# Performance work log

Measured on AMD Instinct MI355X. Metric: run time of the kernel, lower is better.

## Reference

```python
import jax, jax.numpy as jnp
import numpy as np
from jax import lax

IN_CH, OC, NUM_LAYER = 6, 16, 256
ENC_DIM = OC * 4  # 64
DECODE_LEN = 23
FLAT = 5184


def _conv3d(x, w, b):
    # x: (B,C,D,H,W), w: (O,I,3,3,3), padding 1, stride 1
    y = lax.conv_general_dilated(x, w, window_strides=(1, 1, 1),
                                 padding=((1, 1), (1, 1), (1, 1)),
                                 dimension_numbers=('NCDHW', 'OIDHW', 'NCDHW'))
    return y + b[None, :, None, None, None]


def _maxpool(x):
    # MaxPool3d kernel (2,2,1) stride (2,2,1) over (D,H,W)
    return lax.reduce_window(x, -jnp.inf, lax.max,
                             (1, 1, 2, 2, 1), (1, 1, 2, 2, 1), 'VALID')


def setup_inputs() -> dict:
    key = jax.random.key(0)
    ks = jax.random.split(key, 24)
    n = lambda k, s: jax.random.normal(k, s, dtype=jnp.float32) * 0.05
    z = lambda s: jnp.zeros(s, dtype=jnp.float32)
    return {
        'x': jax.random.normal(ks[0], (512, IN_CH, 24, 72, 3), dtype=jnp.float32),
        'w1': n(ks[1], (OC, IN_CH, 3, 3, 3)), 'b1': z((OC,)),
        'w2': n(ks[2], (OC * 2, OC, 3, 3, 3)), 'b2': z((OC * 2,)),
        'w3': n(ks[3], (OC * 4, OC * 2, 3, 3, 3)), 'b3': z((OC * 4,)),
        'wih1': n(ks[4], (NUM_LAYER, ENC_DIM)), 'whh1': n(ks[5], (NUM_LAYER, NUM_LAYER)),
        'bih1': z((NUM_LAYER,)), 'bhh1': z((NUM_LAYER,)),
        'wih2': n(ks[6], (NUM_LAYER, NUM_LAYER)), 'whh2': n(ks[7], (NUM_LAYER, NUM_LAYER)),
        'bih2': z((NUM_LAYER,)), 'bhh2': z((NUM_LAYER,)),
        'w_init_h': n(ks[8], (NUM_LAYER, ENC_DIM)), 'b_init_h': z((NUM_LAYER,)),
        'w_init_h2': n(ks[9], (NUM_LAYER, NUM_LAYER)), 'b_init_h2': z((NUM_LAYER,)),
        'w_fc': n(ks[10], (1, NUM_LAYER)), 'b_fc': z((1,)),
        'w_lin1': n(ks[11], (NUM_LAYER, FLAT)), 'b_lin1': z((NUM_LAYER,)),
        'w_lin2': n(ks[12], (12, NUM_LAYER)), 'b_lin2': z((12,)),
    }


def reference(x, w1, b1, w2, b2, w3, b3,
              wih1, whh1, bih1, bhh1, wih2, whh2, bih2, bhh2,
              w_init_h, b_init_h, w_init_h2, b_init_h2,
              w_fc, b_fc, w_lin1, b_lin1, w_lin2, b_lin2):
    # Encoder: three conv+relu+pool stages (dropout is identity at p=0.0)
    out = _maxpool(jax.nn.relu(_conv3d(x, w1, b1)))
    out = _maxpool(jax.nn.relu(_conv3d(out, w2, b2)))
    out = _maxpool(jax.nn.relu(_conv3d(out, w3, b3)))  # (B, 64, 3, 9, 3)
    out = out.transpose(0, 2, 3, 4, 1)  # (B, D, H, W, C)
    B, C = out.shape[0], out.shape[-1]
    enc = out.reshape(B, -1, C)
    mean_enc = enc.mean(axis=1)  # (B, enc_dim)

    h = mean_enc @ w_init_h.T + b_init_h
    h2 = h @ w_init_h2.T + b_init_h2

    # Precompute the input-to-hidden projection once (constant across steps)
    ih_const = mean_enc @ wih1.T + bih1 + bhh1

    def step(carry, _):
        h, h2 = carry
        h_new = jnp.tanh(ih_const + h @ whh1.T)
        h2_new = jnp.tanh(h_new @ wih2.T + bih2 + h2 @ whh2.T + bhh2)
        pred = h2_new @ w_fc.T + b_fc  # (B, 1)
        return (h_new, h2_new), pred

    _, preds = lax.scan(step, (h, h2), None, length=DECODE_LEN)  # (T, B, 1)
    predictions = preds.transpose(1, 0, 2)  # (B, 23, 1)

    flat = out.reshape(B, -1)  # (B, 5184) in permuted (D,H,W,C) order, same as torch
    out_c = jnp.tanh(flat @ w_lin1.T + b_lin1) @ w_lin2.T + b_lin2  # (B, 12)
    return predictions, out_c
```

## Files before the change

kernel.cpp:

```cpp
#include <hip/hip_runtime.h>
#include <hip/hip_bf16.h>

typedef __attribute__((ext_vector_type(8))) short short8;
typedef __attribute__((ext_vector_type(4))) short short4_t;
typedef __attribute__((ext_vector_type(4))) float floatx4;

#define OFF_B1P   0
#define OFF_B2P   1792
#define OFF_B3P   8960
#define OFF_WIHT  36608
#define OFF_WIH1T 52992
#define OFF_WI2T  69376
#define OFF_WHH1B 134912
#define OFF_WIH2B 167680
#define OFF_WHH2B 200448
#define OFF_WL1P  233216
#define OFF_ME    896768
#define OFF_H     929536
#define OFF_H2    1060608
#define OFF_IHC   1191680
#define OFF_P1    1322752
#define OFF_T1    1322752
#define OFF_Y     2377728
#define OFF_HSEQ  5392384
#define OFF_P2    6631168
#define OFF_P3BF  9285376

#define S2_H 88
#define S2_D 1760
#define S3_H 88
#define S3_D 1760
#define S3_HALF 14080

static __device__ inline short f2bf(float f) {
  union { __hip_bfloat16 h; short s; } u;
  u.h = __float2bfloat16(f);
  return u.s;
}
static __device__ inline float bf2f(short s) {
  union { unsigned u; float f; } v;
  v.u = ((unsigned)(unsigned short)s) << 16;
  return v.f;
}
static __device__ inline float fast_tanh(float x) {
  float e = __expf(2.f * x);
  return __builtin_fmaf(-2.f, __builtin_amdgcn_rcpf(e + 1.f), 1.f);
}

__global__ __launch_bounds__(256) void prep_kernel(
    const float* __restrict__ w1, const float* __restrict__ w2, const float* __restrict__ w3,
    const float* __restrict__ w_init_h, const float* __restrict__ wih1,
    const float* __restrict__ w_init_h2, const float* __restrict__ whh1,
    const float* __restrict__ wih2, const float* __restrict__ whh2,
    float* __restrict__ ws) {
  int i = blockIdx.x * 256 + threadIdx.x;
  if (i < 3584) {
    int j = i & 7, l = (i >> 3) & 63, c = i >> 9;
    int k = c*32 + ((l >> 4) << 3) + j;
    int tap = k >> 3, icp = k & 7, oc = l & 15;
    float v = (tap < 27 && icp < 6) ? w1[(oc*6 + icp)*27 + tap] : 0.f;
    ((__hip_bfloat16*)(ws + OFF_B1P))[i] = __float2bfloat16(v);
    return;
  }
  i -= 3584;
  if (i < 14336) {
    int j = i & 7, l = (i >> 3) & 63, cc = i >> 9;
    int c = cc % 14, nt = cc / 14;
    int k = c*32 + ((l >> 4) << 3) + j;
    int tap = k >> 4, ic = k & 15, oc = nt*16 + (l & 15);
    float v = (tap < 27) ? w2[(oc*16 + ic)*27 + tap] : 0.f;
    ((__hip_bfloat16*)(ws + OFF_B2P))[i] = __float2bfloat16(v);
    return;
  }
  i -= 14336;
  if (i < 55296) {
    int j = i & 7, l = (i >> 3) & 63, cc = i >> 9;
    int c = cc % 27, nt = cc / 27;
    int k = c*32 + ((l >> 4) << 3) + j;
    int ic = k & 31, oc = nt*16 + (l & 15);
    ((__hip_bfloat16*)(ws + OFF_B3P))[i] = __float2bfloat16(w3[(oc*32 + ic)*27 + c]);
    return;
  }
  i -= 55296;
  if (i < 16384) { int t = i & 255, k = i >> 8; ws[OFF_WIHT + i]  = w_init_h[t*64 + k];  return; }
  i -= 16384;
  if (i < 16384) { int t = i & 255, k = i >> 8; ws[OFF_WIH1T + i] = wih1[t*64 + k];      return; }
  i -= 16384;
  if (i < 65536) { int t = i & 255, k = i >> 8; ws[OFF_WI2T + i]  = w_init_h2[t*256 + k]; return; }
  i -= 65536;
  if (i < 65536) { ((__hip_bfloat16*)(ws + OFF_WHH1B))[i] = __float2bfloat16(whh1[i]); return; }
  i -= 65536;
  if (i < 65536) { ((__hip_bfloat16*)(ws + OFF_WIH2B))[i] = __float2bfloat16(wih2[i]); return; }
  i -= 65536;
  if (i < 65536) { ((__hip_bfloat16*)(ws + OFF_WHH2B))[i] = __float2bfloat16(whh2[i]); return; }
}

__global__ __launch_bounds__(256) void conv1_mfma(
    const float* __restrict__ x, const short* __restrict__ b1p,
    const float* __restrict__ bias, short* __restrict__ p1,
    const float* __restrict__ w_lin1, short* __restrict__ wl1p) {
  __shared__ __align__(16) short slab[8 * 74 * 5 * 8];
  int tid = threadIdx.x;
  if (blockIdx.x >= 2048) {
    int i = (blockIdx.x - 2048)*256 + tid;
    int j = i & 7, l = (i >> 3) & 63, cc = i >> 9;
    int c = cc % 162, nt = cc / 162;
    int k = c*32 + ((l >> 4) << 3) + j;
    int n = nt*16 + (l & 15);
    wl1p[i] = f2bf(w_lin1[n*5184 + k]);
    return;
  }
  int b = blockIdx.x >> 2, q = blockIdx.x & 3;
  short8 z8 = {0,0,0,0,0,0,0,0};
  for (int i = tid; i < 2960; i += 256) *(short8*)(slab + i*8) = z8;
  __syncthreads();
  if (tid < 216) {
    int p = tid;
    int h = p / 3, w = p - h*3;
    short* dst0 = slab + ((1 + h)*5 + (1 + w))*8;
    const float* src0 = x + (size_t)b*6*24*216 + p;
    #pragma unroll 1
    for (int dslot = 0; dslot < 8; ++dslot) {
      int d = 6*q - 1 + dslot;
      if ((unsigned)d < 24u) {
        short8 s = z8;
        #pragma unroll
        for (int ic = 0; ic < 6; ++ic)
          s[ic] = f2bf(src0[(ic*24 + d)*216]);
        *(short8*)(dst0 + dslot*74*5*8) = s;
      }
    }
  }
  int lane = tid & 63, wid = tid >> 6;
  int quad = lane >> 4, col = lane & 15;
  short8 bf[7];
  #pragma unroll
  for (int c = 0; c < 7; ++c) bf[c] = *(const short8*)(b1p + (c*64 + lane)*8);
  int tapoff[7];
  #pragma unroll
  for (int c = 0; c < 7; ++c) {
    int tap = c*4 + quad;
    int tt = tap < 27 ? tap : 26;
    int kd = tt/9, rr = tt - kd*9, kh = rr/3, kw = rr - kh*3;
    tapoff[c] = ((kd*74 + kh)*5 + kw)*8;
  }
  float bv = bias[col];
  __syncthreads();
  for (int tile = wid; tile < 81; tile += 4) {
    int m = tile*16 + col;
    int dd = m & 1, dh = (m >> 1) & 1;
    int P = m >> 2;
    int t2 = P/3; int w = P - t2*3;
    int pdl = t2/36; int ph = t2 - pdl*36;
    int base = (((2*pdl + dd)*74 + 2*ph + dh)*5 + w)*8;
    floatx4 acc = {0.f, 0.f, 0.f, 0.f};
    #pragma unroll
    for (int c = 0; c < 7; ++c) {
      short8 af = *(const short8*)(slab + base + tapoff[c]);
      acc = __builtin_amdgcn_mfma_f32_16x16x32_bf16(af, bf[c], acc, 0, 0, 0);
    }
    float v = fmaxf(fmaxf(acc[0], acc[1]), fmaxf(acc[2], acc[3]));
    v = fmaxf(v + bv, 0.f);
    int Pout = q*324 + tile*4 + quad;
    p1[((size_t)b*1296 + Pout)*16 + col] = f2bf(v);
  }
}

__global__ __launch_bounds__(256) void conv2_mfma(
    const short* __restrict__ p1, const short* __restrict__ b2p,
    const float* __restrict__ bias2, short* __restrict__ p2g) {
  __shared__ __align__(16) short slab[14 * S2_D];
  int tid = threadIdx.x;
  int b = blockIdx.x >> 1, qh = blockIdx.x & 1;
  short8 z8 = {0,0,0,0,0,0,0,0};
  for (int i = tid; i < 3080; i += 256) *(short8*)(slab + i*8) = z8;
  __syncthreads();
  for (int i = tid; i < 1440; i += 256) {
    int c8 = i % 6; int r = i / 6; int hr = r % 20; int d = r / 20;
    int hg = 18*qh - 1 + hr;
    if ((unsigned)hg < 36u) {
      short8 v = *(const short8*)(p1 + ((size_t)b*1296 + (d*36 + hg)*3)*16 + c8*8);
      *(short8*)(slab + (d+1)*S2_D + hr*S2_H + 16 + c8*8) = v;
    }
  }
  int lane = tid & 63, wid = tid >> 6;
  int quad = lane >> 4, col = lane & 15;
  short8 bf[2][14];
  #pragma unroll
  for (int nt = 0; nt < 2; ++nt)
    #pragma unroll
    for (int c = 0; c < 14; ++c)
      bf[nt][c] = *(const short8*)(b2p + ((nt*14 + c)*64 + lane)*8);
  int tq = quad >> 1, icoff = (quad & 1) * 8;
  int tapoff[14];
  #pragma unroll
  for (int c = 0; c < 14; ++c) {
    int tap = 2*c + tq; if (tap > 26) tap = 26;
    int kd = tap/9, rr = tap - kd*9, kh = rr/3, kw = rr - kh*3;
    tapoff[c] = kd*S2_D + kh*S2_H + kw*16 + icoff;
  }
  float bv0 = bias2[col], bv1 = bias2[16 + col];
  __syncthreads();
  for (int tile = wid; tile < 41; tile += 4) {
    int m = tile*16 + col; if (m > 647) m = 647;
    int dd = m & 1, dh = (m >> 1) & 1;
    int P = m >> 2;
    int t = P/3; int w = P - t*3;
    int pd = t/9; int phl = t - pd*9;
    int base = (2*pd + dd)*S2_D + (2*phl + dh)*S2_H + w*16;
    floatx4 a0 = {0.f,0.f,0.f,0.f}, a1 = {0.f,0.f,0.f,0.f};
    #pragma unroll
    for (int c = 0; c < 14; ++c) {
      short8 a = *(const short8*)(slab + base + tapoff[c]);
      a0 = __builtin_amdgcn_mfma_f32_16x16x32_bf16(a, bf[0][c], a0, 0, 0, 0);
      a1 = __builtin_amdgcn_mfma_f32_16x16x32_bf16(a, bf[1][c], a1, 0, 0, 0);
    }
    int P2l = tile*4 + quad;
    if (P2l < 162) {
      float v0 = fmaxf(fmaxf(fmaxf(a0[0],a0[1]), fmaxf(a0[2],a0[3])) + bv0, 0.f);
      float v1 = fmaxf(fmaxf(fmaxf(a1[0],a1[1]), fmaxf(a1[2],a1[3])) + bv1, 0.f);
      int t2 = P2l/3; int w2 = P2l - t2*3;
      int pd2 = t2/9; int ph2 = t2 - pd2*9;
      size_t off = ((size_t)b*324 + (pd2*18 + 9*qh + ph2)*3 + w2)*32;
      p2g[off + col] = f2bf(v0);
      p2g[off + 16 + col] = f2bf(v1);
    }
  }
}

__global__ __launch_bounds__(256) void conv3_mfma(
    const short* __restrict__ p2g, const short* __restrict__ b3p,
    const float* __restrict__ bias3,
    short* __restrict__ p3bf, float* __restrict__ me) {
  __shared__ __align__(16) short slab[2 * S3_HALF];
  __shared__ float smean[4][32];
  int tid = threadIdx.x;
  int b = blockIdx.x;
  short8 z8 = {0,0,0,0,0,0,0,0};
  for (int i = tid; i < 3520; i += 256) *(short8*)(slab + i*8) = z8;
  __syncthreads();
  for (int i = tid; i < 1296; i += 256) {
    int c8 = i & 1;
    int hv = (i >> 1) & 1;
    int cell = i >> 2;
    int t = cell/3; int w = cell - t*3;
    int d = t/18; int h = t - d*18;
    short8 v = *(const short8*)(p2g + ((size_t)b*324 + cell)*32 + hv*16 + c8*8);
    *(short8*)(slab + hv*S3_HALF + (d+1)*S3_D + (h+1)*S3_H + (w+1)*16 + c8*8) = v;
  }
  int lane = tid & 63, wid = tid >> 6;
  int quad = lane >> 4, col = lane & 15;
  int ntp = (wid & 1) * 2;
  int tsel = wid >> 1;
  short8 bf[2][27];
  #pragma unroll
  for (int u = 0; u < 2; ++u)
    #pragma unroll
    for (int c = 0; c < 27; ++c)
      bf[u][c] = *(const short8*)(b3p + (((ntp+u)*27 + c)*64 + lane)*8);
  const short* sb = slab + (quad >> 1)*S3_HALF + (quad & 1)*8;
  float bva = bias3[ntp*16 + col], bvb = bias3[(ntp+1)*16 + col];
  float ms0 = 0.f, ms1 = 0.f;
  __syncthreads();
  for (int tile = tsel; tile < 21; tile += 2) {
    int m = tile*16 + col; if (m > 323) m = 323;
    int dd = m & 1, dh = (m >> 1) & 1;
    int P = m >> 2;
    int t = P/3; int w = P - t*3;
    int pd = t/9; int ph = t - pd*9;
    const short* ap = sb + (2*pd + dd)*S3_D + (2*ph + dh)*S3_H + w*16;
    floatx4 a0 = {0.f,0.f,0.f,0.f}, a1 = {0.f,0.f,0.f,0.f};
    #pragma unroll
    for (int c = 0; c < 27; ++c) {
      const int kd = c/9, rr = c - kd*9, kh = rr/3, kw = rr - kh*3;
      short8 a = *(const short8*)(ap + kd*S3_D + kh*S3_H + kw*16);
      a0 = __builtin_amdgcn_mfma_f32_16x16x32_bf16(a, bf[0][c], a0, 0, 0, 0);
      a1 = __builtin_amdgcn_mfma_f32_16x16x32_bf16(a, bf[1][c], a1, 0, 0, 0);
    }
    int Pout = tile*4 + quad;
    if (Pout < 81) {
      float v0 = fmaxf(fmaxf(fmaxf(a0[0],a0[1]), fmaxf(a0[2],a0[3])) + bva, 0.f);
      float v1 = fmaxf(fmaxf(fmaxf(a1[0],a1[1]), fmaxf(a1[2],a1[3])) + bvb, 0.f);
      size_t oi = ((size_t)b*81 + Pout)*64 + ntp*16 + col;
      p3bf[oi] = f2bf(v0);
      p3bf[oi + 16] = f2bf(v1);
      ms0 += v0; ms1 += v1;
    }
  }
  ms0 += __shfl_xor(ms0, 16, 64); ms0 += __shfl_xor(ms0, 32, 64);
  ms1 += __shfl_xor(ms1, 16, 64); ms1 += __shfl_xor(ms1, 32, 64);
  if (lane < 16) { smean[wid][lane] = ms0; smean[wid][16 + lane] = ms1; }
  __syncthreads();
  if (tid < 64) {
    float s = (tid < 32) ? (smean[0][tid] + smean[2][tid])
                         : (smean[1][tid-32] + smean[3][tid-32]);
    me[b*64 + tid] = s * (1.f / 81.f);
  }
}

__global__ __launch_bounds__(256) void init_kernel(
    const float* __restrict__ me, const float* __restrict__ wiht,
    const float* __restrict__ b_init_h, const float* __restrict__ wih1t,
    const float* __restrict__ bih1, const float* __restrict__ bhh1,
    const float* __restrict__ wi2t, const float* __restrict__ b_init_h2,
    float* __restrict__ hout, float* __restrict__ h2out, float* __restrict__ ihcout) {
  __shared__ float sme[8][64];
  __shared__ float shl[8][256];
  int t = threadIdx.x; int bb = blockIdx.x * 8;
  for (int i = t; i < 512; i += 256) {
    int m = i >> 6, c = i & 63;
    sme[m][c] = me[(bb + m)*64 + c];
  }
  __syncthreads();
  float a[8], cc[8];
  float ba = b_init_h[t], bc = bih1[t] + bhh1[t];
  #pragma unroll
  for (int r = 0; r < 8; ++r) { a[r] = ba; cc[r] = bc; }
  #pragma unroll 2
  for (int k = 0; k < 64; ++k) {
    float w1v = wiht[k*256 + t], w2v = wih1t[k*256 + t];
    #pragma unroll
    for (int r = 0; r < 8; ++r) {
      float m = sme[r][k];
      a[r]  += m * w1v;
      cc[r] += m * w2v;
    }
  }
  #pragma unroll
  for (int r = 0; r < 8; ++r) {
    hout[(size_t)(bb + r)*256 + t] = a[r];
    ihcout[(size_t)(bb + r)*256 + t] = cc[r];
    shl[r][t] = a[r];
  }
  __syncthreads();
  float a2[8];
  float b2 = b_init_h2[t];
  #pragma unroll
  for (int r = 0; r < 8; ++r) a2[r] = b2;
  #pragma unroll 2
  for (int k = 0; k < 256; ++k) {
    float wv = wi2t[k*256 + t];
    #pragma unroll
    for (int r = 0; r < 8; ++r) a2[r] += shl[r][k] * wv;
  }
  #pragma unroll
  for (int r = 0; r < 8; ++r) h2out[(size_t)(bb + r)*256 + t] = a2[r];
}

__global__ __launch_bounds__(512) void fusedA(
    const float* __restrict__ hin, const float* __restrict__ ihc,
    const short* __restrict__ whh1b, short* __restrict__ hseq,
    const short* __restrict__ p3bf, const short* __restrict__ wl1p,
    const float* __restrict__ b_lin1, float* __restrict__ t1) {
  __shared__ __align__(16) short hbuf[2][16][264];
  __shared__ __align__(16) short Ab[2][512][8];
  __shared__ __align__(16) short Bb[2][512][8];
  int tid = threadIdx.x;

  if (blockIdx.x >= 32) {
    int sub = tid >> 8, stid = tid & 255;
    int lane = stid & 63, w = stid >> 6;
    int quad = lane >> 4, col = lane & 15;
    int idx = (blockIdx.x - 32)*2 + sub;
    int mt = idx & 7, ntb = (idx >> 3) & 3, kz = idx >> 5;
    int c0 = (kz <= 2) ? kz*22 : 44 + (kz - 2)*20;
    int cn = (kz < 2) ? 22 : ((kz == 7) ? 18 : 20);
    int Nr = cn >> 1;
    int m0 = mt*64;
    floatx4 acc[4];
    #pragma unroll
    for (int t = 0; t < 4; ++t) {
      float bv = (kz == 0) ? b_lin1[ntb*64 + t*16 + col] : 0.f;
      #pragma unroll
      for (int r = 0; r < 4; ++r) acc[t][r] = bv;
    }
    const short* asrc = p3bf + (size_t)(m0 + w*16 + col)*5184 + c0*32 + quad*8;
    const short* bsrc = wl1p + ((size_t)((ntb*4 + w)*162 + c0)*64 + lane)*8;
    short8 ra0 = *(const short8*)asrc;
    short8 ra1 = *(const short8*)(asrc + 32);
    short8 rb0 = *(const short8*)bsrc;
    short8 rb1 = *(const short8*)(bsrc + 512);
    asrc += 64; bsrc += 1024;
    #pragma unroll 1
    for (int r = 0; r < Nr; ++r) {
      *(short8*)&Ab[0][tid][0] = ra0;
      *(short8*)&Ab[1][tid][0] = ra1;
      *(short8*)&Bb[0][tid][0] = rb0;
      *(short8*)&Bb[1][tid][0] = rb1;
      if (r + 1 < Nr) {
        ra0 = *(const short8*)asrc;
        ra1 = *(const short8*)(asrc + 32);
        rb0 = *(const short8*)bsrc;
        rb1 = *(const short8*)(bsrc + 512);
        asrc += 64; bsrc += 1024;
      }
      __syncthreads();
      #pragma unroll
      for (int cc = 0; cc < 2; ++cc) {
        short8 a = *(const short8*)&Ab[cc][sub*256 + w*64 + lane][0];
        #pragma unroll
        for (int t = 0; t < 4; ++t) {
          short8 b = *(const short8*)&Bb[cc][sub*256 + t*64 + lane][0];
          acc[t] = __builtin_amdgcn_mfma_f32_16x16x32_bf16(a, b, acc[t], 0, 0, 0);
        }
      }
      __syncthreads();
    }
    float* to = t1 + (size_t)kz * 131072;
    #pragma unroll
    for (int t = 0; t < 4; ++t)
      #pragma unroll
      for (int r = 0; r < 4; ++r)
        to[(size_t)(m0 + w*16 + quad*4 + r)*256 + ntb*64 + t*16 + col] = acc[t][r];
    return;
  }

  int lane = tid & 63, wid = tid >> 6;
  int quad = lane >> 4, col = lane & 15;
  int bb = blockIdx.x * 16;
  int n0 = wid * 32;
  short8 w1f[2][8];
  #pragma unroll
  for (int t = 0; t < 2; ++t)
    #pragma unroll
    for (int c = 0; c < 8; ++c)
      w1f[t][c] = *(const short8*)(whh1b + (n0 + t*16 + col)*256 + c*32 + quad*8);
  floatx4 ihcr[2];
  #pragma unroll
  for (int t = 0; t < 2; ++t) {
    float4 iv = *(const float4*)(ihc + (size_t)(bb + col)*256 + n0 + t*16 + quad*4);
    ihcr[t][0] = iv.x; ihcr[t][1] = iv.y; ihcr[t][2] = iv.z; ihcr[t][3] = iv.w;
  }
  #pragma unroll
  for (int t = 0; t < 2; ++t)
    #pragma unroll
    for (int c = 0; c < 8; ++c) asm volatile("" : "+v"(w1f[t][c]));

  for (int i = tid; i < 4096; i += 512) {
    int m = i >> 8, k = i & 255;
    hbuf[0][m][k] = f2bf(hin[(size_t)(bb + m)*256 + k]);
  }
  __syncthreads();
  #pragma unroll 1
  for (int i = 0; i < 23; ++i) {
    int cur = i & 1;
    floatx4 a1[2];
    #pragma unroll
    for (int t = 0; t < 2; ++t) {
      a1[t][0] = ihcr[t][0]; a1[t][1] = ihcr[t][1];
      a1[t][2] = ihcr[t][2]; a1[t][3] = ihcr[t][3];
    }
    #pragma unroll
    for (int c = 0; c < 8; ++c) {
      short8 hb = *(const short8*)&hbuf[cur][col][c*32 + quad*8];
      a1[0] = __builtin_amdgcn_mfma_f32_16x16x32_bf16(w1f[0][c], hb, a1[0], 0, 0, 0);
      a1[1] = __builtin_amdgcn_mfma_f32_16x16x32_bf16(w1f[1][c], hb, a1[1], 0, 0, 0);
    }
    #pragma unroll
    for (int t = 0; t < 2; ++t) {
      short4_t pk;
      #pragma unroll
      for (int r = 0; r < 4; ++r) pk[r] = f2bf(fast_tanh(a1[t][r]));
      *(short4_t*)&hbuf[cur ^ 1][col][n0 + t*16 + quad*4] = pk;
      *(short4_t*)(hseq + ((size_t)i*512 + bb + col)*256 + n0 + t*16 + quad*4) = pk;
    }
    __syncthreads();
  }
}

__global__ __launch_bounds__(512) void fusedB(
    const short* __restrict__ hseq, const short* __restrict__ wih2b,
    const float* __restrict__ bih2, const float* __restrict__ bhh2,
    float* __restrict__ yseq,
    const float* __restrict__ t1, const float* __restrict__ w_lin2,
    const float* __restrict__ b_lin2, float* __restrict__ outc) {
  __shared__ __align__(16) short As[64][72];
  __shared__ __align__(16) short Bs[256][72];
  __shared__ float st[16][257];
  int tid = threadIdx.x;

  if (blockIdx.x < 32) {
    int bb = blockIdx.x * 16;
    for (int i = tid; i < 4096; i += 512) {
      int m = i >> 8, k = i & 255;
      size_t i0 = (size_t)(bb + m)*256 + k;
      float s = 0.f;
      #pragma unroll
      for (int z = 0; z < 8; ++z) s += t1[i0 + (size_t)z*131072];
      st[m][k] = fast_tanh(s);
    }
    __syncthreads();
    if (tid < 192) {
      int r = tid / 12, j = tid % 12;
      float s = b_lin2[j];
      #pragma unroll 1
      for (int k = 0; k < 256; ++k) s += st[r][k] * w_lin2[j*256 + k];
      outc[(size_t)(bb + r)*12 + j] = s;
    }
    return;
  }

  int lane = tid & 63, w = tid >> 6;
  int quad = lane >> 4, col = lane & 15;
  int m0 = (blockIdx.x - 32) * 64;
  int n0 = w * 32;
  float bv[2];
  #pragma unroll
  for (int t = 0; t < 2; ++t) {
    int n = n0 + t*16 + col;
    bv[t] = bih2[n] + bhh2[n];
  }
  floatx4 acc[4][2];
  #pragma unroll
  for (int ms = 0; ms < 4; ++ms)
    #pragma unroll
    for (int t = 0; t < 2; ++t)
      #pragma unroll
      for (int r = 0; r < 4; ++r) acc[ms][t][r] = bv[t];
  int arow = tid >> 3, achk = tid & 7;
  #pragma unroll 1
  for (int kr = 0; kr < 256; kr += 64) {
    short8 ra = *(const short8*)(hseq + (size_t)(m0 + arow)*256 + kr + achk*8);
    short8 rb[4];
    #pragma unroll
    for (int p = 0; p < 4; ++p) {
      int idx = p*512 + tid;
      rb[p] = *(const short8*)(wih2b + (size_t)(idx >> 3)*256 + kr + (idx & 7)*8);
    }
    if (kr) __syncthreads();
    *(short8*)&As[arow][achk*8] = ra;
    #pragma unroll
    for (int p = 0; p < 4; ++p) {
      int idx = p*512 + tid;
      *(short8*)&Bs[idx >> 3][(idx & 7)*8] = rb[p];
    }
    __syncthreads();
    #pragma unroll
    for (int cc = 0; cc < 2; ++cc) {
      short8 bfr[2];
      #pragma unroll
      for (int t = 0; t < 2; ++t)
        bfr[t] = *(const short8*)&Bs[n0 + t*16 + col][cc*32 + quad*8];
      #pragma unroll
      for (int ms = 0; ms < 4; ++ms) {
        short8 afr = *(const short8*)&As[ms*16 + col][cc*32 + quad*8];
        acc[ms][0] = __builtin_amdgcn_mfma_f32_16x16x32_bf16(afr, bfr[0], acc[ms][0], 0, 0, 0);
        acc[ms][1] = __builtin_amdgcn_mfma_f32_16x16x32_bf16(afr, bfr[1], acc[ms][1], 0, 0, 0);
      }
    }
  }
  #pragma unroll
  for (int ms = 0; ms < 4; ++ms)
    #pragma unroll
    for (int t = 0; t < 2; ++t)
      #pragma unroll
      for (int r = 0; r < 4; ++r)
        yseq[(size_t)(m0 + ms*16 + quad*4 + r)*256 + n0 + t*16 + col] = acc[ms][t][r];
}

__global__ __launch_bounds__(512) void t_h2(
    const float* __restrict__ h2in, const float* __restrict__ yseq,
    const short* __restrict__ whh2b,
    const float* __restrict__ w_fc, const float* __restrict__ b_fc,
    float* __restrict__ preds) {
  __shared__ __align__(16) short h2buf[2][16][264];
  __shared__ float predsAll[23][8][16];
  int tid = threadIdx.x;
  int lane = tid & 63, wid = tid >> 6;
  int quad = lane >> 4, col = lane & 15;
  int bb = blockIdx.x * 16;
  int n0 = wid * 32;
  short8 w3f[2][8];
  #pragma unroll
  for (int t = 0; t < 2; ++t)
    #pragma unroll
    for (int c = 0; c < 8; ++c)
      w3f[t][c] = *(const short8*)(whh2b + (n0 + t*16 + col)*256 + c*32 + quad*8);
  float4 wfcv[2];
  #pragma unroll
  for (int t = 0; t < 2; ++t)
    wfcv[t] = *(const float4*)(w_fc + n0 + t*16 + quad*4);
  float bfc = b_fc[0];
  #pragma unroll
  for (int t = 0; t < 2; ++t)
    #pragma unroll
    for (int c = 0; c < 8; ++c) asm volatile("" : "+v"(w3f[t][c]));

  for (int i = tid; i < 4096; i += 512) {
    int m = i >> 8, k = i & 255;
    h2buf[0][m][k] = f2bf(h2in[(size_t)(bb + m)*256 + k]);
  }
  __syncthreads();
  #pragma unroll 1
  for (int i = 0; i < 23; ++i) {
    int cur = i & 1;
    float4 yv[2];
    #pragma unroll
    for (int t = 0; t < 2; ++t)
      yv[t] = *(const float4*)(yseq + ((size_t)i*512 + bb + col)*256 + n0 + t*16 + quad*4);
    floatx4 z0 = {0.f,0.f,0.f,0.f}, z1 = {0.f,0.f,0.f,0.f};
    #pragma unroll
    for (int c = 0; c < 8; ++c) {
      short8 gb = *(const short8*)&h2buf[cur][col][c*32 + quad*8];
      z0 = __builtin_amdgcn_mfma_f32_16x16x32_bf16(w3f[0][c], gb, z0, 0, 0, 0);
      z1 = __builtin_amdgcn_mfma_f32_16x16x32_bf16(w3f[1][c], gb, z1, 0, 0, 0);
    }
    float pr = 0.f;
    short4_t o0, o1;
    const float* y0p = (const float*)&yv[0];
    const float* y1p = (const float*)&yv[1];
    const float* wf0 = (const float*)&wfcv[0];
    const float* wf1 = (const float*)&wfcv[1];
    #pragma unroll
    for (int r = 0; r < 4; ++r) {
      float t0 = fast_tanh(z0[r] + y0p[r]);
      float t1 = fast_tanh(z1[r] + y1p[r]);
      o0[r] = f2bf(t0); o1[r] = f2bf(t1);
      pr += t0*wf0[r] + t1*wf1[r];
    }
    *(short4_t*)&h2buf[cur ^ 1][col][n0 + quad*4] = o0;
    *(short4_t*)&h2buf[cur ^ 1][col][n0 + 16 + quad*4] = o1;
    pr += __shfl_xor(pr, 16, 64);
    pr += __shfl_xor(pr, 32, 64);
    if (lane < 16) predsAll[i][wid][lane] = pr;
    __syncthreads();
  }
  if (tid < 16) {
    #pragma unroll 1
    for (int p = 0; p < 23; ++p) {
      float sv = bfc;
      #pragma unroll
      for (int w = 0; w < 8; ++w) sv += predsAll[p][w][tid];
      preds[(size_t)(bb + tid)*23 + p] = sv;
    }
  }
}

extern "C" void kernel_launch(void* const* d_in, const int* in_sizes, int n_in,
                              void* d_out, int out_size, void* d_ws, size_t ws_size,
                              hipStream_t stream) {
  const float* x         = (const float*)d_in[0];
  const float* w1        = (const float*)d_in[1];
  const float* b1        = (const float*)d_in[2];
  const float* w2        = (const float*)d_in[3];
  const float* b2        = (const float*)d_in[4];
  const float* w3        = (const float*)d_in[5];
  const float* b3        = (const float*)d_in[6];
  const float* wih1      = (const float*)d_in[7];
  const float* whh1      = (const float*)d_in[8];
  const float* bih1      = (const float*)d_in[9];
  const float* bhh1      = (const float*)d_in[10];
  const float* wih2      = (const float*)d_in[11];
  const float* whh2      = (const float*)d_in[12];
  const float* bih2      = (const float*)d_in[13];
  const float* bhh2      = (const float*)d_in[14];
  const float* w_init_h  = (const float*)d_in[15];
  const float* b_init_h  = (const float*)d_in[16];
  const float* w_init_h2 = (const float*)d_in[17];
  const float* b_init_h2 = (const float*)d_in[18];
  const float* w_fc      = (const float*)d_in[19];
  const float* b_fc      = (const float*)d_in[20];
  const float* w_lin1    = (const float*)d_in[21];
  const float* b_lin1    = (const float*)d_in[22];
  const float* w_lin2    = (const float*)d_in[23];
  const float* b_lin2    = (const float*)d_in[24];
  float* ws  = (float*)d_ws;
  float* out = (float*)d_out;

  prep_kernel<<<1438, 256, 0, stream>>>(w1, w2, w3, w_init_h, wih1, w_init_h2,
                                        whh1, wih2, whh2, ws);
  conv1_mfma<<<7232, 256, 0, stream>>>(x, (const short*)(ws + OFF_B1P), b1,
                                       (short*)(ws + OFF_P1),
                                       w_lin1, (short*)(ws + OFF_WL1P));
  conv2_mfma<<<1024, 256, 0, stream>>>((const short*)(ws + OFF_P1),
                                       (const short*)(ws + OFF_B2P), b2,
                                       (short*)(ws + OFF_P2));
  conv3_mfma<<<512, 256, 0, stream>>>((const short*)(ws + OFF_P2),
                                      (const short*)(ws + OFF_B3P), b3,
                                      (short*)(ws + OFF_P3BF), ws + OFF_ME);
  init_kernel<<<64, 256, 0, stream>>>(ws + OFF_ME, ws + OFF_WIHT, b_init_h, ws + OFF_WIH1T,
                                      bih1, bhh1, ws + OFF_WI2T, b_init_h2,
                                      ws + OFF_H, ws + OFF_H2, ws + OFF_IHC);
  fusedA<<<160, 512, 0, stream>>>(ws + OFF_H, ws + OFF_IHC,
                                  (const short*)(ws + OFF_WHH1B),
                                  (short*)(ws + OFF_HSEQ),
                                  (const short*)(ws + OFF_P3BF),
                                  (const short*)(ws + OFF_WL1P),
                                  b_lin1, ws + OFF_T1);
  fusedB<<<216, 512, 0, stream>>>((const short*)(ws + OFF_HSEQ),
                                  (const short*)(ws + OFF_WIH2B),
                                  bih2, bhh2, ws + OFF_Y,
                                  ws + OFF_T1, w_lin2, b_lin2, out + 11776);
  t_h2<<<32, 512, 0, stream>>>(ws + OFF_H2, ws + OFF_Y,
                               (const short*)(ws + OFF_WHH2B),
                               w_fc, b_fc, out);
}
```

Measured before the change: 336.3 us.

## Move h2 init GEMM into fusedA as MFMA blocks, store h0 as bf16

The init kernel now computes only h and ihc, with 2 rows per block across 256 blocks, and writes h directly as bf16. The h @ w_init_h2 GEMM moves out of the serial FP32 init kernel into 8 extra bf16 MFMA blocks appended to fusedA, which run alongside the recurrence and lin1 blocks. The aim is to shorten the critical path through init_kernel and to make fusedA's h load a vectorized bf16 copy. The cost is bf16 rounding of h and w_init_h2 in the h2 initialization, plus shared memory aliased through a single pool.

Measured after the change: 296.3 us. 1.14x faster.

```diff
diff --git a/kernel.cpp b/kernel.cpp
--- a/kernel.cpp
+++ b/kernel.cpp
@@ -10,13 +10,13 @@
 #define OFF_B3P   8960
 #define OFF_WIHT  36608
 #define OFF_WIH1T 52992
-#define OFF_WI2T  69376
+#define OFF_WI2B  69376
 #define OFF_WHH1B 134912
 #define OFF_WIH2B 167680
 #define OFF_WHH2B 200448
 #define OFF_WL1P  233216
 #define OFF_ME    896768
-#define OFF_H     929536
+#define OFF_H0BF  929536
 #define OFF_H2    1060608
 #define OFF_IHC   1191680
 #define OFF_P1    1322752
@@ -86,7 +86,7 @@
   i -= 16384;
   if (i < 16384) { int t = i & 255, k = i >> 8; ws[OFF_WIH1T + i] = wih1[t*64 + k];      return; }
   i -= 16384;
-  if (i < 65536) { int t = i & 255, k = i >> 8; ws[OFF_WI2T + i]  = w_init_h2[t*256 + k]; return; }
+  if (i < 65536) { ((__hip_bfloat16*)(ws + OFF_WI2B))[i] = __float2bfloat16(w_init_h2[i]); return; }
   i -= 65536;
   if (i < 65536) { ((__hip_bfloat16*)(ws + OFF_WHH1B))[i] = __float2bfloat16(whh1[i]); return; }
   i -= 65536;
@@ -302,62 +302,97 @@
     const float* __restrict__ me, const float* __restrict__ wiht,
     const float* __restrict__ b_init_h, const float* __restrict__ wih1t,
     const float* __restrict__ bih1, const float* __restrict__ bhh1,
-    const float* __restrict__ wi2t, const float* __restrict__ b_init_h2,
-    float* __restrict__ hout, float* __restrict__ h2out, float* __restrict__ ihcout) {
-  __shared__ float sme[8][64];
-  __shared__ float shl[8][256];
-  int t = threadIdx.x; int bb = blockIdx.x * 8;
-  for (int i = t; i < 512; i += 256) {
-    int m = i >> 6, c = i & 63;
-    sme[m][c] = me[(bb + m)*64 + c];
-  }
-  __syncthreads();
-  float a[8], cc[8];
-  float ba = b_init_h[t], bc = bih1[t] + bhh1[t];
-  #pragma unroll
-  for (int r = 0; r < 8; ++r) { a[r] = ba; cc[r] = bc; }
-  #pragma unroll 2
+    short* __restrict__ h0bf, float* __restrict__ ihcout) {
+  __shared__ float sme[2][64];
+  int t = threadIdx.x; int bb = blockIdx.x * 2;
+  if (t < 128) sme[t >> 6][t & 63] = me[(bb + (t >> 6))*64 + (t & 63)];
+  __syncthreads();
+  float a0 = b_init_h[t], a1 = a0;
+  float c0 = bih1[t] + bhh1[t], c1 = c0;
+  #pragma unroll
   for (int k = 0; k < 64; ++k) {
     float w1v = wiht[k*256 + t], w2v = wih1t[k*256 + t];
-    #pragma unroll
-    for (int r = 0; r < 8; ++r) {
-      float m = sme[r][k];
-      a[r]  += m * w1v;
-      cc[r] += m * w2v;
-    }
-  }
-  #pragma unroll
-  for (int r = 0; r < 8; ++r) {
-    hout[(size_t)(bb + r)*256 + t] = a[r];
-    ihcout[(size_t)(bb + r)*256 + t] = cc[r];
-    shl[r][t] = a[r];
-  }
-  __syncthreads();
-  float a2[8];
-  float b2 = b_init_h2[t];
-  #pragma unroll
-  for (int r = 0; r < 8; ++r) a2[r] = b2;
-  #pragma unroll 2
-  for (int k = 0; k < 256; ++k) {
-    float wv = wi2t[k*256 + t];
-    #pragma unroll
-    for (int r = 0; r < 8; ++r) a2[r] += shl[r][k] * wv;
-  }
-  #pragma unroll
-  for (int r = 0; r < 8; ++r) h2out[(size_t)(bb + r)*256 + t] = a2[r];
+    a0 += sme[0][k]*w1v; a1 += sme[1][k]*w1v;
+    c0 += sme[0][k]*w2v; c1 += sme[1][k]*w2v;
+  }
+  h0bf[(size_t)bb*256 + t]     = f2bf(a0);
+  h0bf[(size_t)(bb+1)*256 + t] = f2bf(a1);
+  ihcout[(size_t)bb*256 + t]     = c0;
+  ihcout[(size_t)(bb+1)*256 + t] = c1;
 }
 
 __global__ __launch_bounds__(512) void fusedA(
-    const float* __restrict__ hin, const float* __restrict__ ihc,
+    const short* __restrict__ h0bf, const float* __restrict__ ihc,
     const short* __restrict__ whh1b, short* __restrict__ hseq,
     const short* __restrict__ p3bf, const short* __restrict__ wl1p,
-    const float* __restrict__ b_lin1, float* __restrict__ t1) {
-  __shared__ __align__(16) short hbuf[2][16][264];
-  __shared__ __align__(16) short Ab[2][512][8];
-  __shared__ __align__(16) short Bb[2][512][8];
+    const float* __restrict__ b_lin1, float* __restrict__ t1,
+    const short* __restrict__ wi2b, const float* __restrict__ b_init_h2,
+    float* __restrict__ h2out) {
+  __shared__ __align__(16) short pool[23040];
   int tid = threadIdx.x;
 
+  if (blockIdx.x >= 160) {
+    short (*As)[72] = (short (*)[72])pool;
+    short (*Bs)[72] = (short (*)[72])(pool + 4608);
+    int lane = tid & 63, w = tid >> 6;
+    int quad = lane >> 4, col = lane & 15;
+    int m0 = (blockIdx.x - 160) * 64;
+    int n0 = w * 32;
+    float bv[2];
+    #pragma unroll
+    for (int t = 0; t < 2; ++t) bv[t] = b_init_h2[n0 + t*16 + col];
+    floatx4 acc[4][2];
+    #pragma unroll
+    for (int ms = 0; ms < 4; ++ms)
+      #pragma unroll
+      for (int t = 0; t < 2; ++t)
+        #pragma unroll
+        for (int r = 0; r < 4; ++r) acc[ms][t][r] = bv[t];
+    int arow = tid >> 3, achk = tid & 7;
+    #pragma unroll 1
+    for (int kr = 0; kr < 256; kr += 64) {
+      short8 ra = *(const short8*)(h0bf + (size_t)(m0 + arow)*256 + kr + achk*8);
+      short8 rb[4];
+      #pragma unroll
+      for (int p = 0; p < 4; ++p) {
+        int idx = p*512 + tid;
+        rb[p] = *(const short8*)(wi2b + (size_t)(idx >> 3)*256 + kr + (idx & 7)*8);
+      }
+      if (kr) __syncthreads();
+      *(short8*)&As[arow][achk*8] = ra;
+      #pragma unroll
+      for (int p = 0; p < 4; ++p) {
+        int idx = p*512 + tid;
+        *(short8*)&Bs[idx >> 3][(idx & 7)*8] = rb[p];
+      }
+      __syncthreads();
+      #pragma unroll
+      for (int cc = 0; cc < 2; ++cc) {
+        short8 bfr[2];
+        #pragma unroll
+        for (int t = 0; t < 2; ++t)
+          bfr[t] = *(const short8*)&Bs[n0 + t*16 + col][cc*32 + quad*8];
+        #pragma unroll
+        for (int ms = 0; ms < 4; ++ms) {
+          short8 afr = *(const short8*)&As[ms*16 + col][cc*32 + quad*8];
+          acc[ms][0] = __builtin_amdgcn_mfma_f32_16x16x32_bf16(afr, bfr[0], acc[ms][0], 0, 0, 0);
+          acc[ms][1] = __builtin_amdgcn_mfma_f32_16x16x32_bf16(afr, bfr[1], acc[ms][1], 0, 0, 0);
+        }
+      }
+    }
+    #pragma unroll
+    for (int ms = 0; ms < 4; ++ms)
+      #pragma unroll
+      for (int t = 0; t < 2; ++t)
+        #pragma unroll
+        for (int r = 0; r < 4; ++r)
+          h2out[(size_t)(m0 + ms*16 + quad*4 + r)*256 + n0 + t*16 + col] = acc[ms][t][r];
+    return;
+  }
+
   if (blockIdx.x >= 32) {
+    short (*Ab)[512][8] = (short (*)[512][8])pool;
+    short (*Bb)[512][8] = (short (*)[512][8])(pool + 8192);
     int sub = tid >> 8, stid = tid & 255;
     int lane = stid & 63, w = stid >> 6;
     int quad = lane >> 4, col = lane & 15;
@@ -415,6 +450,7 @@
     return;
   }
 
+  short (*hbuf)[16][264] = (short (*)[16][264])pool;
   int lane = tid & 63, wid = tid >> 6;
   int quad = lane >> 4, col = lane & 15;
   int bb = blockIdx.x * 16;
@@ -436,9 +472,9 @@
     #pragma unroll
     for (int c = 0; c < 8; ++c) asm volatile("" : "+v"(w1f[t][c]));
 
-  for (int i = tid; i < 4096; i += 512) {
-    int m = i >> 8, k = i & 255;
-    hbuf[0][m][k] = f2bf(hin[(size_t)(bb + m)*256 + k]);
+  {
+    int m = tid >> 5, c = tid & 31;
+    *(short8*)&hbuf[0][m][c*8] = *(const short8*)(h0bf + (size_t)(bb + m)*256 + c*8);
   }
   __syncthreads();
   #pragma unroll 1
@@ -678,15 +714,17 @@
   conv3_mfma<<<512, 256, 0, stream>>>((const short*)(ws + OFF_P2),
                                       (const short*)(ws + OFF_B3P), b3,
                                       (short*)(ws + OFF_P3BF), ws + OFF_ME);
-  init_kernel<<<64, 256, 0, stream>>>(ws + OFF_ME, ws + OFF_WIHT, b_init_h, ws + OFF_WIH1T,
-                                      bih1, bhh1, ws + OFF_WI2T, b_init_h2,
-                                      ws + OFF_H, ws + OFF_H2, ws + OFF_IHC);
-  fusedA<<<160, 512, 0, stream>>>(ws + OFF_H, ws + OFF_IHC,
+  init_kernel<<<256, 256, 0, stream>>>(ws + OFF_ME, ws + OFF_WIHT, b_init_h,
+                                       ws + OFF_WIH1T, bih1, bhh1,
+                                       (short*)(ws + OFF_H0BF), ws + OFF_IHC);
+  fusedA<<<168, 512, 0, stream>>>((const short*)(ws + OFF_H0BF), ws + OFF_IHC,
                                   (const short*)(ws + OFF_WHH1B),
                                   (short*)(ws + OFF_HSEQ),
                                   (const short*)(ws + OFF_P3BF),
                                   (const short*)(ws + OFF_WL1P),
-                                  b_lin1, ws + OFF_T1);
+                                  b_lin1, ws + OFF_T1,
+                                  (const short*)(ws + OFF_WI2B), b_init_h2,
+                                  ws + OFF_H2);
   fusedB<<<216, 512, 0, stream>>>((const short*)(ws + OFF_HSEQ),
                                   (const short*)(ws + OFF_WIH2B),
                                   bih2, bhh2, ws + OFF_Y,
```
